# Optimization experiments

Hardware: AMD Instinct MI355X
Metric: run time of the kernel (lower is better)

The kernel has to match this reference:

```python
import jax, jax.numpy as jnp
import numpy as np

N = 100000   # nodes
E = 1600000  # edges
D_IN = 4
D_H = 128
EPS = 1e-5

def setup_inputs() -> dict:
    key = jax.random.key(0)
    ks = jax.random.split(key, 4)
    x = jax.random.normal(ks[0], (N, D_IN), dtype=jnp.float32)
    edge_index = jax.random.randint(ks[1], (2, E), 0, N, dtype=jnp.int32)
    W0 = jax.random.normal(ks[2], (D_IN, D_H), dtype=jnp.float32) * 0.5
    b0 = jnp.zeros((D_H,), jnp.float32)
    W12 = jax.random.normal(ks[3], (2, D_H, D_H), dtype=jnp.float32) * (1.0 / np.sqrt(D_H))
    b12 = jnp.zeros((2, D_H), jnp.float32)
    gamma = jnp.ones((3, D_H), jnp.float32)   # GraphNorm weight
    beta = jnp.zeros((3, D_H), jnp.float32)   # GraphNorm bias
    alpha = jnp.ones((3, D_H), jnp.float32)   # GraphNorm mean_scale
    return dict(x=x, edge_index=edge_index, W0=W0, b0=b0, W12=W12, b12=b12,
                gamma=gamma, beta=beta, alpha=alpha)

def gcn_conv(x, src, dst, dinv, W, b):
    # PyG GCNConv: linear first, then D^-1/2 (A+I) D^-1/2 aggregation, bias after.
    h = x @ W                                  # [N, d_out]
    coef = dinv[src] * dinv[dst]               # [E]
    msg = h[src] * coef[:, None]               # [E, d_out] gather
    agg = jax.ops.segment_sum(msg, dst, num_segments=N)  # scatter-add
    agg = agg + h * (dinv * dinv)[:, None]     # self-loop contribution
    return agg + b

def graph_norm(x, g, be, a):
    # single-graph GraphNorm: gamma*(x - alpha*mu)/sqrt(E[(x-alpha*mu)^2]+eps)+beta
    mu = x.mean(axis=0)
    xc = x - a * mu
    var = (xc * xc).mean(axis=0)
    return g * xc * jax.lax.rsqrt(var + EPS) + be

def reference(x, edge_index, W0, b0, W12, b12, gamma, beta, alpha):
    src, dst = edge_index[0], edge_index[1]
    # degree with self loops (edge weight 1)
    deg = jax.ops.segment_sum(jnp.ones((E,), x.dtype), dst, num_segments=N) + 1.0
    dinv = jax.lax.rsqrt(deg)
    h = jax.nn.relu(graph_norm(gcn_conv(x, src, dst, dinv, W0, b0),
                               gamma[0], beta[0], alpha[0]))
    for i in range(2):  # fixed small layer loop
        h = jax.nn.relu(graph_norm(gcn_conv(h, src, dst, dinv, W12[i], b12[i]),
                                   gamma[i + 1], beta[i + 1], alpha[i + 1]))
    return h
```

## Files before the change

### kernel.cpp

```cpp
#include <hip/hip_runtime.h>


#define EPS_GN 1e-5f

typedef __attribute__((ext_vector_type(8))) short bf16x8;
typedef __attribute__((ext_vector_type(4))) float f32x4;

__device__ __forceinline__ float blo(unsigned u) { return __uint_as_float(u << 16); }
__device__ __forceinline__ float bhi(unsigned u) { return __uint_as_float(u & 0xffff0000u); }
__device__ __forceinline__ unsigned bf16rne(float f) {
  unsigned u = __float_as_uint(f);
  u += 0x7fff + ((u >> 16) & 1);
  return u >> 16;
}
__device__ __forceinline__ unsigned packbf(float x, float y) {
  return bf16rne(x) | (bf16rne(y) << 16);
}


__global__ __launch_bounds__(256) void k_count_p(const int* __restrict__ dst,
                                                 int* __restrict__ cnt, int E, int N) {
  int p = blockIdx.x & 7;
  int lo = (int)((long long)N * p >> 3), hi = (int)((long long)N * (p + 1) >> 3);
  int stride = (gridDim.x >> 3) * 256;
  for (int e = (blockIdx.x >> 3) * 256 + threadIdx.x; e < E; e += stride) {
    int d = dst[e];
    if (d >= lo && d < hi) atomicAdd(&cnt[d], 1);
  }
}

__global__ __launch_bounds__(256) void k_scan1(const int* __restrict__ cnt,
                                               int* __restrict__ rs,
                                               int* __restrict__ bsum, int N) {
  __shared__ int s[256];
  int t = threadIdx.x;
  int base = blockIdx.x * 1024 + t * 4;
  int c0 = (base + 0 < N) ? ((cnt[base + 0] + 8) & ~7) : 0;
  int c1 = (base + 1 < N) ? ((cnt[base + 1] + 8) & ~7) : 0;
  int c2 = (base + 2 < N) ? ((cnt[base + 2] + 8) & ~7) : 0;
  int c3 = (base + 3 < N) ? ((cnt[base + 3] + 8) & ~7) : 0;
  int tsum = c0 + c1 + c2 + c3;
  s[t] = tsum;
  __syncthreads();
  for (int off = 1; off < 256; off <<= 1) {
    int v = (t >= off) ? s[t - off] : 0;
    __syncthreads();
    s[t] += v;
    __syncthreads();
  }
  int excl = s[t] - tsum;
  if (t == 255) bsum[blockIdx.x] = s[255];
  int e0 = excl, e1 = e0 + c0, e2 = e1 + c1, e3 = e2 + c2;
  if (base + 0 < N) rs[base + 0] = e0;
  if (base + 1 < N) rs[base + 1] = e1;
  if (base + 2 < N) rs[base + 2] = e2;
  if (base + 3 < N) rs[base + 3] = e3;
}

__global__ __launch_bounds__(256) void k_scan2(const int* __restrict__ bsum,
                                               int* __restrict__ boff, int nblk) {
  __shared__ int s[256];
  int t = threadIdx.x;
  int v0 = (t < nblk) ? bsum[t] : 0;
  s[t] = v0;
  __syncthreads();
  for (int off = 1; off < 256; off <<= 1) {
    int v = (t >= off) ? s[t - off] : 0;
    __syncthreads();
    s[t] += v;
    __syncthreads();
  }
  if (t < nblk) boff[t] = s[t] - v0;
}

__global__ __launch_bounds__(256) void k_finalize(const int* __restrict__ cnt,
                                                  const int* __restrict__ boff,
                                                  int* __restrict__ rs,
                                                  int* __restrict__ cursor,
                                                  float* __restrict__ dinv,
                                                  unsigned* __restrict__ Hcb,
                                                  int* __restrict__ csrp, int N, int E,
                                                  int ROWS) {
  __shared__ int sTail;
  int i = blockIdx.x * 256 + threadIdx.x;
  if (i < 64) Hcb[((size_t)(i >> 3) * ROWS + N) * 8 + (i & 7)] = 0u;
  if (i < N) {
    int v = rs[i] + boff[i >> 10];
    int c = cnt[i];
    int pc = (c + 8) & ~7;
    rs[i] = v;
    cursor[i] = v + 1;
    dinv[i] = rsqrtf((float)c + 1.0f);
    csrp[v] = i;
    for (int k = v + 1 + c; k < v + pc; ++k) csrp[k] = N;
    if (i == N - 1) {
      rs[N] = v + pc;
      sTail = v + pc;
    }
  }
  __syncthreads();
  if (blockIdx.x == gridDim.x - 1) {
    int base = sTail;
    for (int k = threadIdx.x; k < 1024; k += 256) csrp[base + k] = N;
  }
}

__global__ __launch_bounds__(256) void k_fill_p(const int* __restrict__ src,
                                                const int* __restrict__ dst,
                                                int* __restrict__ cursor,
                                                int* __restrict__ csrp, int E, int N) {
  int p = blockIdx.x & 7;
  int lo = (int)((long long)N * p >> 3), hi = (int)((long long)N * (p + 1) >> 3);
  int stride = (gridDim.x >> 3) * 256;
  for (int e = (blockIdx.x >> 3) * 256 + threadIdx.x; e < E; e += stride) {
    int d = dst[e];
    if (d >= lo && d < hi) {
      int pos = atomicAdd(&cursor[d], 1);
      csrp[pos] = src[e];
    }
  }
}


__global__ __launch_bounds__(256) void k_wt(const float* __restrict__ W12,
                                            unsigned short* __restrict__ WbT) {
  int o = blockIdx.x * 256 + threadIdx.x;
  int layer = o >> 14, r = o & 16383;
  int n = r >> 7, k = r & 127;
  WbT[o] = (unsigned short)bf16rne(W12[layer * 16384 + k * 128 + n]);
}


__global__ __launch_bounds__(256) void k_gemm0(const float* __restrict__ X,
                                               const float* __restrict__ W,
                                               const float* __restrict__ dinv,
                                               unsigned* __restrict__ Hcb, int N, int ROWS) {
  __shared__ float Ws[4 * 128];
  int t = threadIdx.x;
  if (t < 128) {
    Ws[t] = W[t];
    Ws[128 + t] = W[128 + t];
    Ws[256 + t] = W[256 + t];
    Ws[384 + t] = W[384 + t];
  }
  __syncthreads();
  int r = t >> 6, l = t & 63;
  int row = blockIdx.x * 4 + r;
  if (row >= N) return;
  float4 xv = ((const float4*)X)[row];
  float di = dinv[row];
  int c0 = 2 * l, c1 = 2 * l + 1;
  float v0 = xv.x * Ws[c0] + xv.y * Ws[128 + c0] + xv.z * Ws[256 + c0] + xv.w * Ws[384 + c0];
  float v1 = xv.x * Ws[c1] + xv.y * Ws[128 + c1] + xv.z * Ws[256 + c1] + xv.w * Ws[384 + c1];
  Hcb[((size_t)(l >> 3) * ROWS + row) * 8 + (l & 7)] = packbf(di * v0, di * v1);
}

__global__ __launch_bounds__(256, 4) void k_gemm_mfma(const unsigned* __restrict__ AGGcb,
                                                      const unsigned short* __restrict__ WbT,
                                                      const float* __restrict__ stats,
                                                      const float* __restrict__ bias,
                                                      const float* __restrict__ gamma,
                                                      const float* __restrict__ beta,
                                                      const float* __restrict__ alpha,
                                                      const float* __restrict__ dinv,
                                                      unsigned* __restrict__ Hcb, int N,
                                                      int ROWS, float invN) {
  __shared__ float As[128], Bs[128];
  int t = threadIdx.x;
  if (t < 128) {
    float s1 = stats[t] * invN, s2 = stats[128 + t] * invN;
    float b = bias[t], a = alpha[t], g = gamma[t], be = beta[t];
    float mu = s1 + b;
    float E2 = s2 + 2.f * b * s1 + b * b;
    float var = E2 - (2.f * a - a * a) * mu * mu;
    float A = g * rsqrtf(var + EPS_GN);
    As[t] = A;
    Bs[t] = be - A * a * mu + A * b;
  }
  __syncthreads();
  int wv = t >> 6, l = t & 63;
  int r0 = blockIdx.x * 64 + wv * 16;
  if (r0 >= N) return;
  int m = l & 15, kb = l >> 4;

  f32x4 acc[8];
#pragma unroll
  for (int nt = 0; nt < 8; ++nt) acc[nt] = (f32x4){0.f, 0.f, 0.f, 0.f};

#pragma unroll
  for (int ks = 0; ks < 4; ++ks) {
    int k0 = ks * 32 + kb * 8;
    const uint4* pa = (const uint4*)(AGGcb + ((size_t)(2 * ks + (kb >> 1)) * ROWS + r0 + m) * 8 +
                                     (kb & 1) * 4);
    uint4 a_raw = pa[0];
    float4 A0 = *reinterpret_cast<const float4*>(&As[k0]);
    float4 A1 = *reinterpret_cast<const float4*>(&As[k0 + 4]);
    float4 B0 = *reinterpret_cast<const float4*>(&Bs[k0]);
    float4 B1 = *reinterpret_cast<const float4*>(&Bs[k0 + 4]);
    bf16x8 bf[8];
#pragma unroll
    for (int nt = 0; nt < 8; ++nt)
      bf[nt] = *reinterpret_cast<const bf16x8*>(WbT + (size_t)(nt * 16 + m) * 128 + k0);
    float xr[8] = {blo(a_raw.x), bhi(a_raw.x), blo(a_raw.y), bhi(a_raw.y),
                   blo(a_raw.z), bhi(a_raw.z), blo(a_raw.w), bhi(a_raw.w)};
    float Aa[8] = {A0.x, A0.y, A0.z, A0.w, A1.x, A1.y, A1.z, A1.w};
    float Bb[8] = {B0.x, B0.y, B0.z, B0.w, B1.x, B1.y, B1.z, B1.w};
    bf16x8 af;
#pragma unroll
    for (int j = 0; j < 8; ++j) {
      float v = fmaf(Aa[j], xr[j], Bb[j]);
      v = v > 0.f ? v : 0.f;
      af[j] = (short)bf16rne(v);
    }
#pragma unroll
    for (int nt = 0; nt < 8; ++nt)
      acc[nt] = __builtin_amdgcn_mfma_f32_16x16x32_bf16(af, bf[nt], acc[nt], 0, 0, 0);
  }

  float dn[4];
#pragma unroll
  for (int r = 0; r < 4; ++r) dn[r] = dinv[r0 + kb * 4 + r];
  bool even = (l & 1) == 0;
#pragma unroll
  for (int nt = 0; nt < 8; ++nt) {
#pragma unroll
    for (int r = 0; r < 4; ++r) {
      float v = acc[nt][r] * dn[r];
      float pv = __shfl_xor(v, 1);
      if (even) {
        unsigned word = packbf(v, pv);
        Hcb[((size_t)nt * ROWS + r0 + kb * 4 + r) * 8 + (m >> 1)] = word;
      }
    }
  }
}

__global__ __launch_bounds__(256) void k_gather_cb(const unsigned* __restrict__ Hcb,
                                                   const int* __restrict__ rsp,
                                                   const int* __restrict__ csrp,
                                                   const float* __restrict__ dinv,
                                                   unsigned* __restrict__ AGGcb,
                                                   float* __restrict__ stats, int N, int ROWS) {
  int t = threadIdx.x;
  int wave = t >> 6, lane = t & 63;
  int g = lane >> 4, e = (lane >> 1) & 7, h = lane & 1;
  int p = blockIdx.x & 7;
  const uint4* Hp4 = (const uint4*)(Hcb + (size_t)p * ROWS * 8);
  uint4* Ap4 = (uint4*)(AGGcb + (size_t)p * ROWS * 8);
  int q = blockIdx.x >> 3;
  int nstride = (gridDim.x >> 3) * 16;
  float s1acc[8], s2acc[8];
#pragma unroll
  for (int i = 0; i < 8; ++i) s1acc[i] = s2acc[i] = 0.f;

  for (int n0 = (q * 4 + wave) * 4; n0 < N; n0 += nstride) {
    int n = n0 + g;
    int j0 = rsp[n], j1 = rsp[n + 1];
    int nb = (j1 - j0) >> 3;
    int ml = nb;
    ml = max(ml, __shfl_xor(ml, 16));
    ml = max(ml, __shfl_xor(ml, 32));
    float acc[8];
#pragma unroll
    for (int i = 0; i < 8; ++i) acc[i] = 0.f;

    const int* cp = csrp + j0 + e;
    auto hload = [&](int c, int b) -> uint4 {
      int ce = (b < nb) ? c : N;
      return Hp4[(size_t)ce * 2 + h];
    };
    int c0 = cp[0], c1 = cp[8];
    uint4 hA = hload(c0, 0);
    uint4 hB = hload(c1, 1);
    int c2 = cp[16], c3 = cp[24];
    const int* cpp = cp + 32;

    for (int b = 0; b < ml; b += 2) {
      {
        unsigned uu[4] = {hA.x, hA.y, hA.z, hA.w};
#pragma unroll
        for (int i = 0; i < 4; ++i) {
          acc[2 * i] += blo(uu[i]);
          acc[2 * i + 1] += bhi(uu[i]);
        }
      }
      hA = hload(c2, b + 2);
      c2 = cpp[0];
      if (b + 1 < ml) {
        unsigned uu[4] = {hB.x, hB.y, hB.z, hB.w};
#pragma unroll
        for (int i = 0; i < 4; ++i) {
          acc[2 * i] += blo(uu[i]);
          acc[2 * i + 1] += bhi(uu[i]);
        }
        hB = hload(c3, b + 3);
        c3 = cpp[8];
      }
      cpp += 16;
    }
#pragma unroll
    for (int i = 0; i < 8; ++i) {
      acc[i] += __shfl_xor(acc[i], 2);
      acc[i] += __shfl_xor(acc[i], 4);
      acc[i] += __shfl_xor(acc[i], 8);
    }
    if (e == 0) {
      float dn = dinv[n];
      float v[8];
      uint4 wv;
      unsigned* wp = (unsigned*)&wv;
#pragma unroll
      for (int i = 0; i < 8; ++i) v[i] = acc[i] * dn;
#pragma unroll
      for (int i = 0; i < 4; ++i) wp[i] = packbf(v[2 * i], v[2 * i + 1]);
      Ap4[(size_t)n * 2 + h] = wv;
#pragma unroll
      for (int i = 0; i < 8; ++i) {
        s1acc[i] += v[i];
        s2acc[i] = fmaf(v[i], v[i], s2acc[i]);
      }
    }
  }
#pragma unroll
  for (int i = 0; i < 8; ++i) {
    s1acc[i] += __shfl_xor(s1acc[i], 16);
    s1acc[i] += __shfl_xor(s1acc[i], 32);
    s2acc[i] += __shfl_xor(s2acc[i], 16);
    s2acc[i] += __shfl_xor(s2acc[i], 32);
  }
  __shared__ float sh[4][32];
  if (lane < 2) {
#pragma unroll
    for (int i = 0; i < 8; ++i) {
      sh[wave][h * 8 + i] = s1acc[i];
      sh[wave][16 + h * 8 + i] = s2acc[i];
    }
  }
  __syncthreads();
  if (t < 32) {
    float v = sh[0][t] + sh[1][t] + sh[2][t] + sh[3][t];
    if (t < 16)
      atomicAdd(&stats[p * 16 + t], v);
    else
      atomicAdd(&stats[128 + p * 16 + (t - 16)], v);
  }
}

__global__ __launch_bounds__(256) void k_norm(const unsigned* __restrict__ AGGcb,
                                              const float* __restrict__ stats,
                                              const float* __restrict__ bias,
                                              const float* __restrict__ gamma,
                                              const float* __restrict__ beta,
                                              const float* __restrict__ alpha,
                                              float* __restrict__ OUT, int N, int ROWS,
                                              float invN) {
  int i = blockIdx.x * 256 + threadIdx.x;
  if (i >= N * 32) return;
  int row = i >> 5, c4 = i & 31;
  int blk = c4 >> 2, off = (2 * c4) & 7;
  uint2 u = *(const uint2*)(AGGcb + ((size_t)blk * ROWS + row) * 8 + off);
  float vv[4] = {blo(u.x), bhi(u.x), blo(u.y), bhi(u.y)};
  float ov[4];
#pragma unroll
  for (int j = 0; j < 4; ++j) {
    int c = c4 * 4 + j;
    float s1 = stats[c] * invN, s2 = stats[128 + c] * invN;
    float b = bias[c], a = alpha[c], g = gamma[c], be = beta[c];
    float mu = s1 + b;
    float E2 = s2 + 2.f * b * s1 + b * b;
    float var = E2 - (2.f * a - a * a) * mu * mu;
    float A = g * rsqrtf(var + EPS_GN);
    float B = be - A * a * mu + A * b;
    float o = fmaf(A, vv[j], B);
    ov[j] = o > 0.f ? o : 0.f;
  }
  ((float4*)OUT)[i] = make_float4(ov[0], ov[1], ov[2], ov[3]);
}


extern "C" void kernel_launch(void* const* d_in, const int* in_sizes, int n_in,
                              void* d_out, int out_size, void* d_ws, size_t ws_size,
                              hipStream_t stream) {
  const float* x = (const float*)d_in[0];
  const int* ei = (const int*)d_in[1];
  const float* W0 = (const float*)d_in[2];
  const float* b0 = (const float*)d_in[3];
  const float* W12 = (const float*)d_in[4];
  const float* b12 = (const float*)d_in[5];
  const float* gamma = (const float*)d_in[6];
  const float* beta = (const float*)d_in[7];
  const float* alpha = (const float*)d_in[8];
  float* out = (float*)d_out;

  int N = in_sizes[0] / 4;
  int E = in_sizes[1] / 2;
  int ROWS = N + 1;
  const int* srcArr = ei;
  const int* dstArr = ei + E;

  char* w = (char*)d_ws;
  auto alloc = [&](size_t bytes) {
    char* p = w;
    w += (bytes + 255) & ~(size_t)255;
    return p;
  };
  int* cnt = (int*)alloc((size_t)N * 4);
  float* stats = (float*)alloc(3 * 256 * 4);
  int* rs = (int*)alloc(((size_t)N + 1) * 4);
  int* cursor = (int*)alloc((size_t)N * 4);
  int* bsum = (int*)alloc(512);
  int* boff = (int*)alloc(512);
  unsigned short* WbT = (unsigned short*)alloc(2 * 16384 * 2);
  int* csrp = (int*)alloc(((size_t)E + 8 * (size_t)N + 2048) * 4);
  float* dinv = (float*)alloc((size_t)N * 4);
  unsigned* Hcb = (unsigned*)alloc((size_t)ROWS * 64 * 4);
  unsigned* AGGcb = (unsigned*)alloc((size_t)ROWS * 64 * 4);

  size_t zlen = (size_t)((char*)stats - (char*)cnt) + 3 * 256 * 4;
  hipMemsetAsync(cnt, 0, zlen, stream);

  int nblk = (N + 1023) / 1024;
  k_wt<<<128, 256, 0, stream>>>(W12, WbT);
  k_count_p<<<2048, 256, 0, stream>>>(dstArr, cnt, E, N);
  k_scan1<<<nblk, 256, 0, stream>>>(cnt, rs, bsum, N);
  k_scan2<<<1, 256, 0, stream>>>(bsum, boff, nblk);
  k_finalize<<<(N + 255) / 256, 256, 0, stream>>>(cnt, boff, rs, cursor, dinv, Hcb, csrp, N, E,
                                                  ROWS);
  k_fill_p<<<2048, 256, 0, stream>>>(srcArr, dstArr, cursor, csrp, E, N);

  float invN = 1.0f / (float)N;
  int gGemm = (N + 63) / 64;

  k_gemm0<<<(N + 3) / 4, 256, 0, stream>>>(x, W0, dinv, Hcb, N, ROWS);
  k_gather_cb<<<2048, 256, 0, stream>>>(Hcb, rs, csrp, dinv, AGGcb, stats, N, ROWS);
  k_gemm_mfma<<<gGemm, 256, 0, stream>>>(AGGcb, WbT, stats, b0, gamma, beta, alpha, dinv, Hcb, N,
                                         ROWS, invN);
  k_gather_cb<<<2048, 256, 0, stream>>>(Hcb, rs, csrp, dinv, AGGcb, stats + 256, N, ROWS);
  k_gemm_mfma<<<gGemm, 256, 0, stream>>>(AGGcb, WbT + 16384, stats + 256, b12, gamma + 128,
                                         beta + 128, alpha + 128, dinv, Hcb, N, ROWS, invN);
  k_gather_cb<<<2048, 256, 0, stream>>>(Hcb, rs, csrp, dinv, AGGcb, stats + 512, N, ROWS);
  k_norm<<<(N * 32 + 255) / 256, 256, 0, stream>>>(AGGcb, stats + 512, b12 + 128, gamma + 256,
                                                   beta + 256, alpha + 256, out, N, ROWS, invN);
}
```

Before: 696.8 us.

## Switch intermediate storage from bf16 to fp16 with packed-half aggregation

Replaces bf16 storage of node features, weights and aggregates with fp16. The gather-sum in the aggregation kernel now accumulates in packed half2 instead of unpacking to fp32, and the MFMA uses the f16 variant. CSR column indices are pre-scaled to byte offsets so the gather address needs no multiply. This is meant to cut ALU work in the aggregation inner loop, at the cost of fp16 range and precision for accumulating sums over many neighbors.

```diff
diff --git a/kernel.cpp b/kernel.cpp
--- a/kernel.cpp
+++ b/kernel.cpp
@@ -3,18 +3,16 @@
 
 #define EPS_GN 1e-5f
 
-typedef __attribute__((ext_vector_type(8))) short bf16x8;
+typedef __attribute__((ext_vector_type(8))) _Float16 f16x8;
+typedef __attribute__((ext_vector_type(2))) _Float16 f16x2;
 typedef __attribute__((ext_vector_type(4))) float f32x4;
 
-__device__ __forceinline__ float blo(unsigned u) { return __uint_as_float(u << 16); }
-__device__ __forceinline__ float bhi(unsigned u) { return __uint_as_float(u & 0xffff0000u); }
-__device__ __forceinline__ unsigned bf16rne(float f) {
-  unsigned u = __float_as_uint(f);
-  u += 0x7fff + ((u >> 16) & 1);
-  return u >> 16;
-}
-__device__ __forceinline__ unsigned packbf(float x, float y) {
-  return bf16rne(x) | (bf16rne(y) << 16);
+template <typename T, typename U>
+__device__ __forceinline__ T bc(U u) {
+  return __builtin_bit_cast(T, u);
+}
+__device__ __forceinline__ unsigned pkh(float x, float y) {
+  return bc<unsigned>(__builtin_amdgcn_cvt_pkrtz(x, y));
 }
 
 
@@ -83,6 +81,7 @@
                                                   int ROWS) {
   __shared__ int sTail;
   int i = blockIdx.x * 256 + threadIdx.x;
+  int NB = N * 32;
   if (i < 64) Hcb[((size_t)(i >> 3) * ROWS + N) * 8 + (i & 7)] = 0u;
   if (i < N) {
     int v = rs[i] + boff[i >> 10];
@@ -91,8 +90,8 @@
     rs[i] = v;
     cursor[i] = v + 1;
     dinv[i] = rsqrtf((float)c + 1.0f);
-    csrp[v] = i;
-    for (int k = v + 1 + c; k < v + pc; ++k) csrp[k] = N;
+    csrp[v] = i * 32;
+    for (int k = v + 1 + c; k < v + pc; ++k) csrp[k] = NB;
     if (i == N - 1) {
       rs[N] = v + pc;
       sTail = v + pc;
@@ -101,7 +100,7 @@
   __syncthreads();
   if (blockIdx.x == gridDim.x - 1) {
     int base = sTail;
-    for (int k = threadIdx.x; k < 1024; k += 256) csrp[base + k] = N;
+    for (int k = threadIdx.x; k < 1024; k += 256) csrp[base + k] = NB;
   }
 }
 
@@ -116,18 +115,18 @@
     int d = dst[e];
     if (d >= lo && d < hi) {
       int pos = atomicAdd(&cursor[d], 1);
-      csrp[pos] = src[e];
+      csrp[pos] = src[e] << 5;
     }
   }
 }
 
 
 __global__ __launch_bounds__(256) void k_wt(const float* __restrict__ W12,
-                                            unsigned short* __restrict__ WbT) {
+                                            _Float16* __restrict__ WbT) {
   int o = blockIdx.x * 256 + threadIdx.x;
   int layer = o >> 14, r = o & 16383;
   int n = r >> 7, k = r & 127;
-  WbT[o] = (unsigned short)bf16rne(W12[layer * 16384 + k * 128 + n]);
+  WbT[o] = (_Float16)W12[layer * 16384 + k * 128 + n];
 }
 
 
@@ -152,11 +151,11 @@
   int c0 = 2 * l, c1 = 2 * l + 1;
   float v0 = xv.x * Ws[c0] + xv.y * Ws[128 + c0] + xv.z * Ws[256 + c0] + xv.w * Ws[384 + c0];
   float v1 = xv.x * Ws[c1] + xv.y * Ws[128 + c1] + xv.z * Ws[256 + c1] + xv.w * Ws[384 + c1];
-  Hcb[((size_t)(l >> 3) * ROWS + row) * 8 + (l & 7)] = packbf(di * v0, di * v1);
+  Hcb[((size_t)(l >> 3) * ROWS + row) * 8 + (l & 7)] = pkh(di * v0, di * v1);
 }
 
 __global__ __launch_bounds__(256, 4) void k_gemm_mfma(const unsigned* __restrict__ AGGcb,
-                                                      const unsigned short* __restrict__ WbT,
+                                                      const _Float16* __restrict__ WbT,
                                                       const float* __restrict__ stats,
                                                       const float* __restrict__ bias,
                                                       const float* __restrict__ gamma,
@@ -197,24 +196,35 @@
     float4 A1 = *reinterpret_cast<const float4*>(&As[k0 + 4]);
     float4 B0 = *reinterpret_cast<const float4*>(&Bs[k0]);
     float4 B1 = *reinterpret_cast<const float4*>(&Bs[k0 + 4]);
-    bf16x8 bf[8];
+    f16x8 bf[8];
 #pragma unroll
     for (int nt = 0; nt < 8; ++nt)
-      bf[nt] = *reinterpret_cast<const bf16x8*>(WbT + (size_t)(nt * 16 + m) * 128 + k0);
-    float xr[8] = {blo(a_raw.x), bhi(a_raw.x), blo(a_raw.y), bhi(a_raw.y),
-                   blo(a_raw.z), bhi(a_raw.z), blo(a_raw.w), bhi(a_raw.w)};
+      bf[nt] = *reinterpret_cast<const f16x8*>(WbT + (size_t)(nt * 16 + m) * 128 + k0);
+    unsigned uu[4] = {a_raw.x, a_raw.y, a_raw.z, a_raw.w};
+    float xr[8];
+#pragma unroll
+    for (int i = 0; i < 4; ++i) {
+      f16x2 hp = bc<f16x2>(uu[i]);
+      xr[2 * i] = (float)hp[0];
+      xr[2 * i + 1] = (float)hp[1];
+    }
     float Aa[8] = {A0.x, A0.y, A0.z, A0.w, A1.x, A1.y, A1.z, A1.w};
     float Bb[8] = {B0.x, B0.y, B0.z, B0.w, B1.x, B1.y, B1.z, B1.w};
-    bf16x8 af;
+    float xs[8];
 #pragma unroll
     for (int j = 0; j < 8; ++j) {
       float v = fmaf(Aa[j], xr[j], Bb[j]);
-      v = v > 0.f ? v : 0.f;
-      af[j] = (short)bf16rne(v);
-    }
+      xs[j] = v > 0.f ? v : 0.f;
+    }
+    uint4 au;
+    au.x = pkh(xs[0], xs[1]);
+    au.y = pkh(xs[2], xs[3]);
+    au.z = pkh(xs[4], xs[5]);
+    au.w = pkh(xs[6], xs[7]);
+    f16x8 af = bc<f16x8>(au);
 #pragma unroll
     for (int nt = 0; nt < 8; ++nt)
-      acc[nt] = __builtin_amdgcn_mfma_f32_16x16x32_bf16(af, bf[nt], acc[nt], 0, 0, 0);
+      acc[nt] = __builtin_amdgcn_mfma_f32_16x16x32_f16(af, bf[nt], acc[nt], 0, 0, 0);
   }
 
   float dn[4];
@@ -228,7 +238,7 @@
       float v = acc[nt][r] * dn[r];
       float pv = __shfl_xor(v, 1);
       if (even) {
-        unsigned word = packbf(v, pv);
+        unsigned word = pkh(v, pv);
         Hcb[((size_t)nt * ROWS + r0 + kb * 4 + r) * 8 + (m >> 1)] = word;
       }
     }
@@ -245,8 +255,10 @@
   int wave = t >> 6, lane = t & 63;
   int g = lane >> 4, e = (lane >> 1) & 7, h = lane & 1;
   int p = blockIdx.x & 7;
-  const uint4* Hp4 = (const uint4*)(Hcb + (size_t)p * ROWS * 8);
+  const unsigned char* HpB = (const unsigned char*)Hcb + (size_t)p * ROWS * 32;
   uint4* Ap4 = (uint4*)(AGGcb + (size_t)p * ROWS * 8);
+  int NB = N * 32;
+  int ho = h * 16;
   int q = blockIdx.x >> 3;
   int nstride = (gridDim.x >> 3) * 16;
   float s1acc[8], s2acc[8];
@@ -260,14 +272,14 @@
     int ml = nb;
     ml = max(ml, __shfl_xor(ml, 16));
     ml = max(ml, __shfl_xor(ml, 32));
-    float acc[8];
-#pragma unroll
-    for (int i = 0; i < 8; ++i) acc[i] = 0.f;
+    f16x2 acc[4];
+#pragma unroll
+    for (int i = 0; i < 4; ++i) acc[i] = (f16x2){(_Float16)0, (_Float16)0};
 
     const int* cp = csrp + j0 + e;
     auto hload = [&](int c, int b) -> uint4 {
-      int ce = (b < nb) ? c : N;
-      return Hp4[(size_t)ce * 2 + h];
+      int ce = (b < nb) ? c : NB;
+      return *(const uint4*)(HpB + (unsigned)(ce + ho));
     };
     int c0 = cp[0], c1 = cp[8];
     uint4 hA = hload(c0, 0);
@@ -276,43 +288,40 @@
     const int* cpp = cp + 32;
 
     for (int b = 0; b < ml; b += 2) {
-      {
-        unsigned uu[4] = {hA.x, hA.y, hA.z, hA.w};
-#pragma unroll
-        for (int i = 0; i < 4; ++i) {
-          acc[2 * i] += blo(uu[i]);
-          acc[2 * i + 1] += bhi(uu[i]);
-        }
-      }
+      acc[0] += bc<f16x2>(hA.x);
+      acc[1] += bc<f16x2>(hA.y);
+      acc[2] += bc<f16x2>(hA.z);
+      acc[3] += bc<f16x2>(hA.w);
       hA = hload(c2, b + 2);
       c2 = cpp[0];
       if (b + 1 < ml) {
-        unsigned uu[4] = {hB.x, hB.y, hB.z, hB.w};
-#pragma unroll
-        for (int i = 0; i < 4; ++i) {
-          acc[2 * i] += blo(uu[i]);
-          acc[2 * i + 1] += bhi(uu[i]);
-        }
+        acc[0] += bc<f16x2>(hB.x);
+        acc[1] += bc<f16x2>(hB.y);
+        acc[2] += bc<f16x2>(hB.z);
+        acc[3] += bc<f16x2>(hB.w);
         hB = hload(c3, b + 3);
         c3 = cpp[8];
       }
       cpp += 16;
     }
 #pragma unroll
-    for (int i = 0; i < 8; ++i) {
-      acc[i] += __shfl_xor(acc[i], 2);
-      acc[i] += __shfl_xor(acc[i], 4);
-      acc[i] += __shfl_xor(acc[i], 8);
+    for (int i = 0; i < 4; ++i) {
+      acc[i] += bc<f16x2>((unsigned)__shfl_xor(bc<int>(acc[i]), 2));
+      acc[i] += bc<f16x2>((unsigned)__shfl_xor(bc<int>(acc[i]), 4));
+      acc[i] += bc<f16x2>((unsigned)__shfl_xor(bc<int>(acc[i]), 8));
     }
     if (e == 0) {
       float dn = dinv[n];
       float v[8];
+#pragma unroll
+      for (int i = 0; i < 4; ++i) {
+        v[2 * i] = (float)acc[i][0] * dn;
+        v[2 * i + 1] = (float)acc[i][1] * dn;
+      }
       uint4 wv;
       unsigned* wp = (unsigned*)&wv;
 #pragma unroll
-      for (int i = 0; i < 8; ++i) v[i] = acc[i] * dn;
-#pragma unroll
-      for (int i = 0; i < 4; ++i) wp[i] = packbf(v[2 * i], v[2 * i + 1]);
+      for (int i = 0; i < 4; ++i) wp[i] = pkh(v[2 * i], v[2 * i + 1]);
       Ap4[(size_t)n * 2 + h] = wv;
 #pragma unroll
       for (int i = 0; i < 8; ++i) {
@@ -359,7 +368,8 @@
   int row = i >> 5, c4 = i & 31;
   int blk = c4 >> 2, off = (2 * c4) & 7;
   uint2 u = *(const uint2*)(AGGcb + ((size_t)blk * ROWS + row) * 8 + off);
-  float vv[4] = {blo(u.x), bhi(u.x), blo(u.y), bhi(u.y)};
+  f16x2 p0 = bc<f16x2>(u.x), p1 = bc<f16x2>(u.y);
+  float vv[4] = {(float)p0[0], (float)p0[1], (float)p1[0], (float)p1[1]};
   float ov[4];
 #pragma unroll
   for (int j = 0; j < 4; ++j) {
@@ -410,7 +420,7 @@
   int* cursor = (int*)alloc((size_t)N * 4);
   int* bsum = (int*)alloc(512);
   int* boff = (int*)alloc(512);
-  unsigned short* WbT = (unsigned short*)alloc(2 * 16384 * 2);
+  _Float16* WbT = (_Float16*)alloc(2 * 16384 * 2);
   int* csrp = (int*)alloc(((size_t)E + 8 * (size_t)N + 2048) * 4);
   float* dinv = (float*)alloc((size_t)N * 4);
   unsigned* Hcb = (unsigned*)alloc((size_t)ROWS * 64 * 4);
```

New measurement: 609.8 us. 12.5% less time.
